# Kernel tuning notes

Hardware: AMD Instinct MI355X
Metric: run time of the kernel (lower is better)

The kernel has to match this reference:

```python
import jax, jax.numpy as jnp
import numpy as np

VOX = 64      # vox_size
KS = 21       # smooth_ks (odd -> 'SAME' == pad ks//2)
SIGMA = 3.0   # smooth_sigma


def smoothing_kernel():
    # normalized 1D gaussian used separably along the 3 voxel axes
    x = jnp.arange(KS, dtype=jnp.float32) - (KS - 1) / 2.0
    g = jnp.exp(-(x * x) / (2.0 * SIGMA * SIGMA))
    return g / g.sum()


def pc_voxels(pc, size):
    """Trilinear scatter of points in [-0.5,0.5]^3 into a [B,size,size,size] grid."""
    B, N, _ = pc.shape
    g = (pc + 0.5) * (size - 1)            # grid coords
    fl = jnp.floor(g)
    idx = fl.astype(jnp.int32)             # [B,N,3] lower corner
    frac = g - fl                          # trilinear fractions
    # 8 corner offsets in {0,1}^3
    offs = jnp.array([[(i >> 2) & 1, (i >> 1) & 1, i & 1] for i in range(8)], dtype=jnp.int32)
    pos = idx[:, :, None, :] + offs[None, None]                       # [B,N,8,3]
    w = jnp.prod(jnp.where(offs[None, None].astype(bool),
                           frac[:, :, None, :], 1.0 - frac[:, :, None, :]), axis=-1)  # [B,N,8]
    inb = jnp.all((pos >= 0) & (pos < size), axis=-1)
    w = jnp.where(inb, w, 0.0)
    posc = jnp.clip(pos, 0, size - 1)
    # voxel layout vox[b, z, y, x]; pc columns are (x, y, z)
    flat = posc[..., 2] * (size * size) + posc[..., 1] * size + posc[..., 0]
    vox = jnp.zeros((B, size * size * size), pc.dtype)
    vox = vox.at[jnp.arange(B)[:, None, None], flat].add(w)
    return jnp.clip(vox.reshape(B, size, size, size), 0.0, 1.0)


def voxels_smooth(v, g1d, scale):
    """Separable 3D Gaussian smoothing + per-batch scale, clamped to [0,1]."""
    x = v[:, None]  # NCDHW, C=1
    ks = g1d.shape[0]
    for kshape in ((1, 1, ks, 1, 1), (1, 1, 1, ks, 1), (1, 1, 1, 1, ks)):
        x = jax.lax.conv_general_dilated(
            x, g1d.reshape(kshape), (1, 1, 1), 'SAME',
            dimension_numbers=('NCDHW', 'OIDHW', 'NCDHW'))
    x = x[:, 0] * scale[:, None, None, None]
    return jnp.clip(x, 0.0, 1.0)


def drc_prob(v):
    """DRC ray-termination probabilities along depth (axis 1)."""
    trans = jnp.cumprod(1.0 - v, axis=1)                                   # [B,D,H,W]
    tshift = jnp.concatenate([jnp.ones_like(trans[:, :1]), trans[:, :-1]], axis=1)
    stop = v * tshift                                                      # stop at voxel d
    esc = trans[:, -1:]                                                    # ray escapes
    return jnp.concatenate([stop, esc], axis=1)                            # [B,D+1,H,W]


def reference(pc, rotation, scale):
    pc_t = jnp.einsum('bni,bji->bnj', pc, rotation)   # camera transform: pc @ R^T
    vox = pc_voxels(pc_t, VOX)
    sm = voxels_smooth(vox, smoothing_kernel(), scale)
    prob = drc_prob(sm)
    proj = prob[:, :-1].sum(1)[:, ::-1, :]            # sum over depth, flip rows
    return proj


def setup_inputs() -> dict:
    key = jax.random.key(0)
    k1, k2, k3 = jax.random.split(key, 3)
    B, N = 32, 65536
    pc = jax.random.uniform(k1, (B, N, 3), jnp.float32) - 0.5   # points in [-0.5, 0.5]
    q, _ = jnp.linalg.qr(jax.random.normal(k2, (B, 3, 3), jnp.float32))  # random rotations
    scale = 0.5 + jax.random.uniform(k3, (B,), jnp.float32)
    return {"pc": pc, "rotation": q, "scale": scale}
```

## Files before the change

kernel.cpp:

```cpp
#include <hip/hip_runtime.h>

#define NB    32
#define NP    65536
#define SZ    64
#define SZ3   (SZ * SZ * SZ)
#define KS    21
#define HALF  10
#define NBIN  65
#define CAP   2048
#define FXS   960.0f

typedef _Float16 half8_t __attribute__((ext_vector_type(8)));
typedef _Float16 half4_t __attribute__((ext_vector_type(4)));
typedef float    f32x4_t __attribute__((ext_vector_type(4)));

__device__ __forceinline__ int swz(int row, int col) {
    return (row << 6) + ((((col >> 3) ^ (row & 7))) << 3) + (col & 7);
}

__device__ __forceinline__ void weights_reg(float* w) {
    float sum = 0.0f;
#pragma unroll
    for (int k = 0; k < KS; ++k) {
        float d = (float)k - (float)HALF;
        w[k] = expf(-d * d / 18.0f);
        sum += w[k];
    }
#pragma unroll
    for (int k = 0; k < KS; ++k) w[k] /= sum;
}

__device__ __forceinline__ void fma4(float4& a, float t, const float4& v) {
    a.x = fmaf(t, v.x, a.x); a.y = fmaf(t, v.y, a.y);
    a.z = fmaf(t, v.z, a.z); a.w = fmaf(t, v.w, a.w);
}

__device__ __forceinline__ unsigned pack_fx(float g) {
    float c = fminf(fmaxf(g, -2.0f), 65.0f);
    return (unsigned)__float2uint_rn((c + 2.0f) * FXS);
}

__global__ void fill_kernel(const float* __restrict__ pc,
                            const float* __restrict__ rot,
                            int* __restrict__ cur,
                            uint2* __restrict__ binned,
                            _Float16* __restrict__ Gg) {
    __shared__ int h[4][NBIN];
    __shared__ int woff[4][NBIN];
    __shared__ int lbase[NBIN];
    int base = blockIdx.x * 1024;
    int b = base >> 16;
    int wv = threadIdx.x >> 6;
    for (int i = threadIdx.x; i < 4 * NBIN; i += 256) h[i / NBIN][i % NBIN] = 0;
    __syncthreads();
    const float* R = rot + b * 9;
    const float4* p4 = (const float4*)(pc + (size_t)base * 3);
    float4 f0 = p4[threadIdx.x * 3 + 0];
    float4 f1 = p4[threadIdx.x * 3 + 1];
    float4 f2 = p4[threadIdx.x * 3 + 2];
    float px[4] = {f0.x, f0.w, f1.z, f2.y};
    float py[4] = {f0.y, f1.x, f1.w, f2.z};
    float pz[4] = {f0.z, f1.y, f2.x, f2.w};
    uint2 pk[4];
    int bin[4], lpos[4];
#pragma unroll
    for (int j = 0; j < 4; ++j) {
        float g0 = (R[0] * px[j] + R[1] * py[j] + R[2] * pz[j] + 0.5f) * 63.0f;
        float g1 = (R[3] * px[j] + R[4] * py[j] + R[5] * pz[j] + 0.5f) * 63.0f;
        float g2 = (R[6] * px[j] + R[7] * py[j] + R[8] * pz[j] + 0.5f) * 63.0f;
        int i2 = (int)floorf(g2);
        bin[j] = (i2 >= -1 && i2 <= 63) ? i2 + 1 : -1;
        pk[j] = make_uint2(pack_fx(g0) | (pack_fx(g1) << 16), pack_fx(g2));
        if (bin[j] >= 0) lpos[j] = atomicAdd(&h[wv][bin[j]], 1);
    }
    __syncthreads();
    if (threadIdx.x < NBIN) {
        int t = threadIdx.x;
        int s0 = h[0][t], s1 = h[1][t], s2 = h[2][t], s3 = h[3][t];
        int tot = s0 + s1 + s2 + s3;
        lbase[t] = tot ? atomicAdd(&cur[b * NBIN + t], tot) : 0;
        woff[0][t] = 0; woff[1][t] = s0; woff[2][t] = s0 + s1; woff[3][t] = s0 + s1 + s2;
    }
    __syncthreads();
#pragma unroll
    for (int j = 0; j < 4; ++j)
        if (bin[j] >= 0) {
            int pos = lbase[bin[j]] + woff[wv][bin[j]] + lpos[j];
            if (pos < CAP)
                binned[(size_t)(b * NBIN + bin[j]) * CAP + pos] = pk[j];
        }
    if (blockIdx.x == 0) {
        float w[KS];
        weights_reg(w);
        for (int i = threadIdx.x; i < 4096; i += 256) {
            int d = (i >> 6) - (i & 63) + HALF;
            Gg[i] = ((unsigned)d < (unsigned)KS) ? (_Float16)w[d] : (_Float16)0.0f;
        }
    }
}

__global__ void __launch_bounds__(64) splat_blur(const uint2* __restrict__ binned,
                                                 const int* __restrict__ cur,
                                                 const _Float16* __restrict__ Gg,
                                                 _Float16* __restrict__ vox) {
    __shared__ __align__(16) _Float16 Ay[65 * 64];
    __shared__ __align__(16) _Float16 Bx[65 * 64];
    int lane = threadIdx.x;
    int idx = blockIdx.x;
    int b = idx >> 6;
    int z = (idx + (b << 3)) & 63;
    int q = lane >> 4, c = lane & 15;

    {
        int4 z4 = {0, 0, 0, 0};
        int4* a4 = (int4*)Ay;
        int4* b4 = (int4*)Bx;
        for (int i = lane; i < 65 * 64 * 2 / 16; i += 64) { a4[i] = z4; b4[i] = z4; }
    }

    half8_t gf[4][2];
#pragma unroll
    for (int ni = 0; ni < 4; ++ni)
#pragma unroll
        for (int h = 0; h < 2; ++h)
            gf[ni][h] = *(const half8_t*)&Gg[(ni * 16 + c) * 64 + h * 32 + q * 8];

    int c0 = min(cur[b * NBIN + z],     CAP);
    int c1 = min(cur[b * NBIN + z + 1], CAP);
    const uint2* s0 = binned + (size_t)(b * NBIN + z) * CAP;
    const uint2* s1 = binned + (size_t)(b * NBIN + z + 1) * CAP;
    int n = c0 + c1;

    f32x4_t acc[4][4];
#pragma unroll
    for (int mi = 0; mi < 4; ++mi)
#pragma unroll
        for (int ni = 0; ni < 4; ++ni) acc[mi][ni] = (f32x4_t){0.f, 0.f, 0.f, 0.f};

    int iters = (n + 63) >> 6;
    uint2 nxt = make_uint2(0u, 0u);
    if (lane < n) nxt = (lane < c0) ? s0[lane] : s1[lane - c0];
    for (int it = 0; it < iters; ++it) {
        uint2 pk = nxt;
        int ni2 = (it + 1) * 64 + lane;
        nxt = make_uint2(0u, 0u);
        if (ni2 < n) nxt = (ni2 < c0) ? s0[ni2] : s1[ni2 - c0];

        float gx = (float)(pk.x & 0xffffu) * (1.0f / FXS) - 2.0f;
        float gy = (float)(pk.x >> 16)     * (1.0f / FXS) - 2.0f;
        float gz = (float)(pk.y & 0xffffu) * (1.0f / FXS) - 2.0f;
        float f0 = floorf(gx), f1 = floorf(gy);
        int   i0 = (int)f0,    i1 = (int)f1;
        float r0 = gx - f0,    r1f = gy - f1;
        float az = fmaxf(0.0f, 1.0f - fabsf(gz - (float)z));
        int ylo = ((unsigned)i1       < 64u) ? i1       : 64;
        int yhi = ((unsigned)(i1 + 1) < 64u) ? (i1 + 1) : 64;
        int xlo = ((unsigned)i0       < 64u) ? i0       : 64;
        int xhi = ((unsigned)(i0 + 1) < 64u) ? (i0 + 1) : 64;
        Ay[swz(ylo, lane)] = (_Float16)(az * (1.0f - r1f));
        Ay[swz(yhi, lane)] = (_Float16)(az * r1f);
        Bx[swz(xlo, lane)] = (_Float16)(1.0f - r0);
        Bx[swz(xhi, lane)] = (_Float16)r0;
#pragma unroll
        for (int h = 0; h < 2; ++h) {
            half8_t af[4], bf[4];
#pragma unroll
            for (int mi = 0; mi < 4; ++mi)
                af[mi] = *(const half8_t*)&Ay[swz(mi * 16 + c, h * 32 + q * 8)];
#pragma unroll
            for (int ni = 0; ni < 4; ++ni)
                bf[ni] = *(const half8_t*)&Bx[swz(ni * 16 + c, h * 32 + q * 8)];
#pragma unroll
            for (int mi = 0; mi < 4; ++mi)
#pragma unroll
                for (int ni = 0; ni < 4; ++ni)
                    acc[mi][ni] = __builtin_amdgcn_mfma_f32_16x16x32_f16(
                        af[mi], bf[ni], acc[mi][ni], 0, 0, 0);
        }
        Ay[swz(ylo, lane)] = (_Float16)0.0f;
        Ay[swz(yhi, lane)] = (_Float16)0.0f;
        Bx[swz(xlo, lane)] = (_Float16)0.0f;
        Bx[swz(xhi, lane)] = (_Float16)0.0f;
    }

    asm volatile("" ::: "memory");
    _Float16* P = Ay;
    _Float16* T = Bx;

#pragma unroll
    for (int mi = 0; mi < 4; ++mi)
#pragma unroll
        for (int ni = 0; ni < 4; ++ni)
#pragma unroll
            for (int r = 0; r < 4; ++r)
                P[swz(mi * 16 + q * 4 + r, ni * 16 + c)] =
                    (_Float16)fminf(fmaxf(acc[mi][ni][r], 0.0f), 1.0f);
    asm volatile("" ::: "memory");

    f32x4_t a2[4][4];
#pragma unroll
    for (int mi = 0; mi < 4; ++mi)
#pragma unroll
        for (int ni = 0; ni < 4; ++ni) a2[mi][ni] = (f32x4_t){0.f, 0.f, 0.f, 0.f};
#pragma unroll
    for (int h = 0; h < 2; ++h) {
        half8_t af[4];
#pragma unroll
        for (int mi = 0; mi < 4; ++mi)
            af[mi] = *(const half8_t*)&P[swz(mi * 16 + c, h * 32 + q * 8)];
#pragma unroll
        for (int mi = 0; mi < 4; ++mi)
#pragma unroll
            for (int ni = 0; ni < 4; ++ni)
                a2[mi][ni] = __builtin_amdgcn_mfma_f32_16x16x32_f16(
                    af[mi], gf[ni][h], a2[mi][ni], 0, 0, 0);
    }
    asm volatile("" ::: "memory");

#pragma unroll
    for (int mi = 0; mi < 4; ++mi)
#pragma unroll
        for (int ni = 0; ni < 4; ++ni) {
            half4_t pkd;
#pragma unroll
            for (int r = 0; r < 4; ++r) pkd[r] = (_Float16)a2[mi][ni][r];
            *(half4_t*)&T[swz(ni * 16 + c, mi * 16 + q * 4)] = pkd;
        }
    asm volatile("" ::: "memory");

    f32x4_t a3[4][4];
#pragma unroll
    for (int mi = 0; mi < 4; ++mi)
#pragma unroll
        for (int ni = 0; ni < 4; ++ni) a3[mi][ni] = (f32x4_t){0.f, 0.f, 0.f, 0.f};
#pragma unroll
    for (int h = 0; h < 2; ++h) {
        half8_t bf[4];
#pragma unroll
        for (int ni = 0; ni < 4; ++ni)
            bf[ni] = *(const half8_t*)&T[swz(ni * 16 + c, h * 32 + q * 8)];
#pragma unroll
        for (int mi = 0; mi < 4; ++mi)
#pragma unroll
            for (int ni = 0; ni < 4; ++ni)
                a3[mi][ni] = __builtin_amdgcn_mfma_f32_16x16x32_f16(
                    gf[mi][h], bf[ni], a3[mi][ni], 0, 0, 0);
    }

    _Float16* dst = vox + ((size_t)b << 18) + ((size_t)z << 12);
#pragma unroll
    for (int mi = 0; mi < 4; ++mi)
#pragma unroll
        for (int ni = 0; ni < 4; ++ni)
#pragma unroll
            for (int r = 0; r < 4; ++r)
                dst[((mi * 16 + q * 4 + r) << 6) + ni * 16 + c] = (_Float16)a3[mi][ni][r];
}

__global__ void convz_drc_kernel(const _Float16* __restrict__ in,
                                 const float* __restrict__ scale,
                                 float* __restrict__ out) {
    __shared__ float sraw[640 + SZ * SZ + 640];
    __shared__ float c[SZ * SZ];
    __shared__ float segS[4][64], segT[4][64];
    float* s = sraw + 640;
    int b = blockIdx.x >> 6, y = blockIdx.x & 63;

    for (int i = threadIdx.x; i < 640; i += 256) {
        sraw[i] = 0.0f;
        sraw[640 + SZ * SZ + i] = 0.0f;
    }
    const _Float16* base = in + ((size_t)b << 18) + (y << 6);
#pragma unroll
    for (int g = 0; g < 4; ++g) {
        int cell = g * 256 + threadIdx.x;
        int z = cell >> 4, xc = (cell & 15) << 2;
        half4_t v = *(const half4_t*)&base[((size_t)z << 12) + xc];
        float4 f = make_float4((float)v[0], (float)v[1], (float)v[2], (float)v[3]);
        *(float4*)&s[(z << 6) + xc] = f;
    }
    __syncthreads();

    float w[KS];
    weights_reg(w);

    {
        int z0 = (threadIdx.x >> 4) << 2;
        int xc = (threadIdx.x & 15) << 2;
        float4 a0 = {0,0,0,0}, a1 = {0,0,0,0}, a2 = {0,0,0,0}, a3 = {0,0,0,0};
#pragma unroll
        for (int d = 0; d < 24; ++d) {
            int zz = z0 - HALF + d;
            float4 v = *(const float4*)&s[(zz << 6) + xc];
            if (d <= 20)           fma4(a0, w[d],     v);
            if (d >= 1 && d <= 21) fma4(a1, w[d - 1], v);
            if (d >= 2 && d <= 22) fma4(a2, w[d - 2], v);
            if (d >= 3)            fma4(a3, w[d - 3], v);
        }
        *(float4*)&c[((z0 + 0) << 6) + xc] = a0;
        *(float4*)&c[((z0 + 1) << 6) + xc] = a1;
        *(float4*)&c[((z0 + 2) << 6) + xc] = a2;
        *(float4*)&c[((z0 + 3) << 6) + xc] = a3;
    }
    __syncthreads();

    {
        int x = threadIdx.x & 63, seg = threadIdx.x >> 6;
        float sc = scale[b];
        float trans = 1.0f, sum = 0.0f;
#pragma unroll
        for (int zz = 0; zz < 16; ++zz) {
            int z = seg * 16 + zz;
            float v = fminf(fmaxf(c[(z << 6) + x] * sc, 0.0f), 1.0f);
            sum += v * trans;
            trans *= 1.0f - v;
        }
        segS[seg][x] = sum;
        segT[seg][x] = trans;
    }
    __syncthreads();
    if (threadIdx.x < 64) {
        int x = threadIdx.x;
        float t = 1.0f, S = 0.0f;
#pragma unroll
        for (int sgi = 0; sgi < 4; ++sgi) { S += segS[sgi][x] * t; t *= segT[sgi][x]; }
        out[(b << 12) + ((63 - y) << 6) + x] = S;
    }
}

extern "C" void kernel_launch(void* const* d_in, const int* in_sizes, int n_in,
                              void* d_out, int out_size, void* d_ws, size_t ws_size,
                              hipStream_t stream) {
    const float* pc    = (const float*)d_in[0];
    const float* rot   = (const float*)d_in[1];
    const float* scale = (const float*)d_in[2];
    float* out = (float*)d_out;

    _Float16* vox    = (_Float16*)d_ws;
    uint2*    binned = (uint2*)((char*)d_ws + (size_t)NB * SZ3 * sizeof(_Float16));
    _Float16* Gg     = (_Float16*)((char*)binned + (size_t)NB * NBIN * CAP * sizeof(uint2));
    int*      cur    = (int*)((char*)Gg + 64 * 64 * sizeof(_Float16));

    hipMemsetAsync(cur, 0, NB * NBIN * sizeof(int), stream);

    fill_kernel     <<<NB * NP / 1024, 256, 0, stream>>>(pc, rot, cur, binned, Gg);
    splat_blur      <<<NB * SZ, 64, 0, stream>>>(binned, cur, Gg, vox);
    convz_drc_kernel<<<NB * SZ, 256, 0, stream>>>(vox, scale, out);
}
```

Baseline: 126.2 us.

## Split splat_blur z-slice across two waves by binning points per y-half

Points are now binned by (z, y-half), so each z-slice block runs two wavefronts, each doing the splat MFMA outer-product over its 32-row half of y. The blur stages are split the same way and synchronised through shared memory. The change also deepens the point prefetch to two iterations and reorders z processing to start from the centre outwards. This trades duplicated binning of points that straddle the y=32 boundary and extra barriers for twice the wave parallelism and half the per-wave MFMA work in the serial splat loop. The smaller CAP2 raises overflow risk if bins are dense.

```diff
diff --git a/kernel.cpp b/kernel.cpp
--- a/kernel.cpp
+++ b/kernel.cpp
@@ -6,8 +6,8 @@
 #define SZ3   (SZ * SZ * SZ)
 #define KS    21
 #define HALF  10
-#define NBIN  65
-#define CAP   2048
+#define NBIN2 130
+#define CAP2  1280
 #define FXS   960.0f
 
 typedef _Float16 half8_t __attribute__((ext_vector_type(8)));
@@ -45,13 +45,13 @@
                             int* __restrict__ cur,
                             uint2* __restrict__ binned,
                             _Float16* __restrict__ Gg) {
-    __shared__ int h[4][NBIN];
-    __shared__ int woff[4][NBIN];
-    __shared__ int lbase[NBIN];
+    __shared__ int h[4][NBIN2];
+    __shared__ int woff[4][NBIN2];
+    __shared__ int lbase[NBIN2];
     int base = blockIdx.x * 1024;
     int b = base >> 16;
     int wv = threadIdx.x >> 6;
-    for (int i = threadIdx.x; i < 4 * NBIN; i += 256) h[i / NBIN][i % NBIN] = 0;
+    for (int i = threadIdx.x; i < 4 * NBIN2; i += 256) h[i / NBIN2][i % NBIN2] = 0;
     __syncthreads();
     const float* R = rot + b * 9;
     const float4* p4 = (const float4*)(pc + (size_t)base * 3);
@@ -62,33 +62,46 @@
     float py[4] = {f0.y, f1.x, f1.w, f2.z};
     float pz[4] = {f0.z, f1.y, f2.x, f2.w};
     uint2 pk[4];
-    int bin[4], lpos[4];
+    int bin0[4], bin1[4], lp0[4], lp1[4];
 #pragma unroll
     for (int j = 0; j < 4; ++j) {
         float g0 = (R[0] * px[j] + R[1] * py[j] + R[2] * pz[j] + 0.5f) * 63.0f;
         float g1 = (R[3] * px[j] + R[4] * py[j] + R[5] * pz[j] + 0.5f) * 63.0f;
         float g2 = (R[6] * px[j] + R[7] * py[j] + R[8] * pz[j] + 0.5f) * 63.0f;
         int i2 = (int)floorf(g2);
-        bin[j] = (i2 >= -1 && i2 <= 63) ? i2 + 1 : -1;
+        int i1 = (int)floorf(g1);
+        bool zv = (i2 >= -1 && i2 <= 63);
+        int h0 = ((unsigned)i1       < 64u) ? (i1 >> 5)       : -1;
+        int h1 = ((unsigned)(i1 + 1) < 64u) ? ((i1 + 1) >> 5) : -1;
+        if (h1 == h0) h1 = -1;
+        bin0[j] = (zv && h0 >= 0) ? ((i2 + 1) * 2 + h0) : -1;
+        bin1[j] = (zv && h1 >= 0) ? ((i2 + 1) * 2 + h1) : -1;
         pk[j] = make_uint2(pack_fx(g0) | (pack_fx(g1) << 16), pack_fx(g2));
-        if (bin[j] >= 0) lpos[j] = atomicAdd(&h[wv][bin[j]], 1);
-    }
-    __syncthreads();
-    if (threadIdx.x < NBIN) {
+        if (bin0[j] >= 0) lp0[j] = atomicAdd(&h[wv][bin0[j]], 1);
+        if (bin1[j] >= 0) lp1[j] = atomicAdd(&h[wv][bin1[j]], 1);
+    }
+    __syncthreads();
+    if (threadIdx.x < NBIN2) {
         int t = threadIdx.x;
         int s0 = h[0][t], s1 = h[1][t], s2 = h[2][t], s3 = h[3][t];
         int tot = s0 + s1 + s2 + s3;
-        lbase[t] = tot ? atomicAdd(&cur[b * NBIN + t], tot) : 0;
+        lbase[t] = tot ? atomicAdd(&cur[b * NBIN2 + t], tot) : 0;
         woff[0][t] = 0; woff[1][t] = s0; woff[2][t] = s0 + s1; woff[3][t] = s0 + s1 + s2;
     }
     __syncthreads();
 #pragma unroll
-    for (int j = 0; j < 4; ++j)
-        if (bin[j] >= 0) {
-            int pos = lbase[bin[j]] + woff[wv][bin[j]] + lpos[j];
-            if (pos < CAP)
-                binned[(size_t)(b * NBIN + bin[j]) * CAP + pos] = pk[j];
-        }
+    for (int j = 0; j < 4; ++j) {
+        if (bin0[j] >= 0) {
+            int pos = lbase[bin0[j]] + woff[wv][bin0[j]] + lp0[j];
+            if (pos < CAP2)
+                binned[(size_t)(b * NBIN2 + bin0[j]) * CAP2 + pos] = pk[j];
+        }
+        if (bin1[j] >= 0) {
+            int pos = lbase[bin1[j]] + woff[wv][bin1[j]] + lp1[j];
+            if (pos < CAP2)
+                binned[(size_t)(b * NBIN2 + bin1[j]) * CAP2 + pos] = pk[j];
+        }
+    }
     if (blockIdx.x == 0) {
         float w[KS];
         weights_reg(w);
@@ -99,52 +112,65 @@
     }
 }
 
-__global__ void __launch_bounds__(64) splat_blur(const uint2* __restrict__ binned,
-                                                 const int* __restrict__ cur,
-                                                 const _Float16* __restrict__ Gg,
-                                                 _Float16* __restrict__ vox) {
-    __shared__ __align__(16) _Float16 Ay[65 * 64];
-    __shared__ __align__(16) _Float16 Bx[65 * 64];
-    int lane = threadIdx.x;
+__global__ void __launch_bounds__(128) splat_blur(const uint2* __restrict__ binned,
+                                                  const int* __restrict__ cur,
+                                                  const _Float16* __restrict__ Gg,
+                                                  _Float16* __restrict__ vox) {
+    __shared__ __align__(16) char smem[25088];
+    int tid = threadIdx.x;
+    int w = tid >> 6, lane = tid & 63;
     int idx = blockIdx.x;
     int b = idx >> 6;
-    int z = (idx + (b << 3)) & 63;
+    int k = (idx + (b << 3)) & 63;
+    int z = (k & 1) ? (31 - (k >> 1)) : (32 + (k >> 1));
     int q = lane >> 4, c = lane & 15;
+
+    _Float16* Ay = (_Float16*)(smem + w * 4224);
+    _Float16* Bx = (_Float16*)(smem + 8448 + w * 8320);
+    _Float16* P  = (_Float16*)smem;
+    _Float16* T  = (_Float16*)(smem + 8448);
 
     {
         int4 z4 = {0, 0, 0, 0};
         int4* a4 = (int4*)Ay;
+        for (int i = lane; i < 4224 / 16; i += 64) a4[i] = z4;
         int4* b4 = (int4*)Bx;
-        for (int i = lane; i < 65 * 64 * 2 / 16; i += 64) { a4[i] = z4; b4[i] = z4; }
+        for (int i = lane; i < 8320 / 16; i += 64) b4[i] = z4;
     }
 
     half8_t gf[4][2];
 #pragma unroll
     for (int ni = 0; ni < 4; ++ni)
 #pragma unroll
-        for (int h = 0; h < 2; ++h)
-            gf[ni][h] = *(const half8_t*)&Gg[(ni * 16 + c) * 64 + h * 32 + q * 8];
-
-    int c0 = min(cur[b * NBIN + z],     CAP);
-    int c1 = min(cur[b * NBIN + z + 1], CAP);
-    const uint2* s0 = binned + (size_t)(b * NBIN + z) * CAP;
-    const uint2* s1 = binned + (size_t)(b * NBIN + z + 1) * CAP;
+        for (int hh = 0; hh < 2; ++hh)
+            gf[ni][hh] = *(const half8_t*)&Gg[(ni * 16 + c) * 64 + hh * 32 + q * 8];
+
+    int c0 = min(cur[b * NBIN2 + 2 * z + w],       CAP2);
+    int c1 = min(cur[b * NBIN2 + 2 * (z + 1) + w], CAP2);
+    const uint2* s0 = binned + (size_t)(b * NBIN2 + 2 * z + w) * CAP2;
+    const uint2* s1 = binned + (size_t)(b * NBIN2 + 2 * (z + 1) + w) * CAP2;
     int n = c0 + c1;
 
-    f32x4_t acc[4][4];
-#pragma unroll
-    for (int mi = 0; mi < 4; ++mi)
-#pragma unroll
-        for (int ni = 0; ni < 4; ++ni) acc[mi][ni] = (f32x4_t){0.f, 0.f, 0.f, 0.f};
+    f32x4_t acc[2][4];
+#pragma unroll
+    for (int ml = 0; ml < 2; ++ml)
+#pragma unroll
+        for (int ni = 0; ni < 4; ++ni) acc[ml][ni] = (f32x4_t){0.f, 0.f, 0.f, 0.f};
 
     int iters = (n + 63) >> 6;
-    uint2 nxt = make_uint2(0u, 0u);
-    if (lane < n) nxt = (lane < c0) ? s0[lane] : s1[lane - c0];
+    uint2 nxtA = make_uint2(0u, 0u), nxtB = make_uint2(0u, 0u);
+    {
+        int i0g = lane;
+        if (i0g < n) nxtA = (i0g < c0) ? s0[i0g] : s1[i0g - c0];
+        int i1g = 64 + lane;
+        if (i1g < n) nxtB = (i1g < c0) ? s0[i1g] : s1[i1g - c0];
+    }
     for (int it = 0; it < iters; ++it) {
-        uint2 pk = nxt;
-        int ni2 = (it + 1) * 64 + lane;
-        nxt = make_uint2(0u, 0u);
-        if (ni2 < n) nxt = (ni2 < c0) ? s0[ni2] : s1[ni2 - c0];
+        uint2 pk = nxtA;
+        nxtA = nxtB;
+        nxtB = make_uint2(0u, 0u);
+        int ni2 = (it + 2) * 64 + lane;
+        if (ni2 < n) nxtB = (ni2 < c0) ? s0[ni2] : s1[ni2 - c0];
 
         float gx = (float)(pk.x & 0xffffu) * (1.0f / FXS) - 2.0f;
         float gy = (float)(pk.x >> 16)     * (1.0f / FXS) - 2.0f;
@@ -153,108 +179,106 @@
         int   i0 = (int)f0,    i1 = (int)f1;
         float r0 = gx - f0,    r1f = gy - f1;
         float az = fmaxf(0.0f, 1.0f - fabsf(gz - (float)z));
-        int ylo = ((unsigned)i1       < 64u) ? i1       : 64;
-        int yhi = ((unsigned)(i1 + 1) < 64u) ? (i1 + 1) : 64;
+        int rlo = i1 - (w << 5), rhi = i1 + 1 - (w << 5);
+        int alo = ((unsigned)rlo < 32u) ? rlo : 32;
+        int ahi = ((unsigned)rhi < 32u) ? rhi : 32;
         int xlo = ((unsigned)i0       < 64u) ? i0       : 64;
         int xhi = ((unsigned)(i0 + 1) < 64u) ? (i0 + 1) : 64;
-        Ay[swz(ylo, lane)] = (_Float16)(az * (1.0f - r1f));
-        Ay[swz(yhi, lane)] = (_Float16)(az * r1f);
+        Ay[swz(alo, lane)] = (_Float16)(az * (1.0f - r1f));
+        Ay[swz(ahi, lane)] = (_Float16)(az * r1f);
         Bx[swz(xlo, lane)] = (_Float16)(1.0f - r0);
         Bx[swz(xhi, lane)] = (_Float16)r0;
 #pragma unroll
-        for (int h = 0; h < 2; ++h) {
-            half8_t af[4], bf[4];
-#pragma unroll
-            for (int mi = 0; mi < 4; ++mi)
-                af[mi] = *(const half8_t*)&Ay[swz(mi * 16 + c, h * 32 + q * 8)];
+        for (int hh = 0; hh < 2; ++hh) {
+            half8_t af[2], bf[4];
+#pragma unroll
+            for (int ml = 0; ml < 2; ++ml)
+                af[ml] = *(const half8_t*)&Ay[swz(ml * 16 + c, hh * 32 + q * 8)];
 #pragma unroll
             for (int ni = 0; ni < 4; ++ni)
-                bf[ni] = *(const half8_t*)&Bx[swz(ni * 16 + c, h * 32 + q * 8)];
-#pragma unroll
-            for (int mi = 0; mi < 4; ++mi)
+                bf[ni] = *(const half8_t*)&Bx[swz(ni * 16 + c, hh * 32 + q * 8)];
+#pragma unroll
+            for (int ml = 0; ml < 2; ++ml)
 #pragma unroll
                 for (int ni = 0; ni < 4; ++ni)
-                    acc[mi][ni] = __builtin_amdgcn_mfma_f32_16x16x32_f16(
-                        af[mi], bf[ni], acc[mi][ni], 0, 0, 0);
-        }
-        Ay[swz(ylo, lane)] = (_Float16)0.0f;
-        Ay[swz(yhi, lane)] = (_Float16)0.0f;
+                    acc[ml][ni] = __builtin_amdgcn_mfma_f32_16x16x32_f16(
+                        af[ml], bf[ni], acc[ml][ni], 0, 0, 0);
+        }
+        Ay[swz(alo, lane)] = (_Float16)0.0f;
+        Ay[swz(ahi, lane)] = (_Float16)0.0f;
         Bx[swz(xlo, lane)] = (_Float16)0.0f;
         Bx[swz(xhi, lane)] = (_Float16)0.0f;
     }
 
-    asm volatile("" ::: "memory");
-    _Float16* P = Ay;
-    _Float16* T = Bx;
-
-#pragma unroll
-    for (int mi = 0; mi < 4; ++mi)
+    __syncthreads();
+
+#pragma unroll
+    for (int ml = 0; ml < 2; ++ml)
 #pragma unroll
         for (int ni = 0; ni < 4; ++ni)
 #pragma unroll
             for (int r = 0; r < 4; ++r)
-                P[swz(mi * 16 + q * 4 + r, ni * 16 + c)] =
-                    (_Float16)fminf(fmaxf(acc[mi][ni][r], 0.0f), 1.0f);
-    asm volatile("" ::: "memory");
-
-    f32x4_t a2[4][4];
-#pragma unroll
-    for (int mi = 0; mi < 4; ++mi)
-#pragma unroll
-        for (int ni = 0; ni < 4; ++ni) a2[mi][ni] = (f32x4_t){0.f, 0.f, 0.f, 0.f};
-#pragma unroll
-    for (int h = 0; h < 2; ++h) {
-        half8_t af[4];
-#pragma unroll
-        for (int mi = 0; mi < 4; ++mi)
-            af[mi] = *(const half8_t*)&P[swz(mi * 16 + c, h * 32 + q * 8)];
-#pragma unroll
-        for (int mi = 0; mi < 4; ++mi)
+                P[swz((w << 5) + ml * 16 + q * 4 + r, ni * 16 + c)] =
+                    (_Float16)fminf(fmaxf(acc[ml][ni][r], 0.0f), 1.0f);
+    __syncthreads();
+
+    f32x4_t a2[2][4];
+#pragma unroll
+    for (int ml = 0; ml < 2; ++ml)
+#pragma unroll
+        for (int ni = 0; ni < 4; ++ni) a2[ml][ni] = (f32x4_t){0.f, 0.f, 0.f, 0.f};
+#pragma unroll
+    for (int hh = 0; hh < 2; ++hh) {
+        half8_t af[2];
+#pragma unroll
+        for (int ml = 0; ml < 2; ++ml)
+            af[ml] = *(const half8_t*)&P[swz(((w << 1) + ml) * 16 + c, hh * 32 + q * 8)];
+#pragma unroll
+        for (int ml = 0; ml < 2; ++ml)
 #pragma unroll
             for (int ni = 0; ni < 4; ++ni)
-                a2[mi][ni] = __builtin_amdgcn_mfma_f32_16x16x32_f16(
-                    af[mi], gf[ni][h], a2[mi][ni], 0, 0, 0);
-    }
-    asm volatile("" ::: "memory");
-
-#pragma unroll
-    for (int mi = 0; mi < 4; ++mi)
+                a2[ml][ni] = __builtin_amdgcn_mfma_f32_16x16x32_f16(
+                    af[ml], gf[ni][hh], a2[ml][ni], 0, 0, 0);
+    }
+#pragma unroll
+    for (int ml = 0; ml < 2; ++ml)
 #pragma unroll
         for (int ni = 0; ni < 4; ++ni) {
             half4_t pkd;
 #pragma unroll
-            for (int r = 0; r < 4; ++r) pkd[r] = (_Float16)a2[mi][ni][r];
-            *(half4_t*)&T[swz(ni * 16 + c, mi * 16 + q * 4)] = pkd;
-        }
-    asm volatile("" ::: "memory");
-
-    f32x4_t a3[4][4];
-#pragma unroll
-    for (int mi = 0; mi < 4; ++mi)
-#pragma unroll
-        for (int ni = 0; ni < 4; ++ni) a3[mi][ni] = (f32x4_t){0.f, 0.f, 0.f, 0.f};
-#pragma unroll
-    for (int h = 0; h < 2; ++h) {
+            for (int r = 0; r < 4; ++r) pkd[r] = (_Float16)a2[ml][ni][r];
+            *(half4_t*)&T[swz(ni * 16 + c, ((w << 1) + ml) * 16 + q * 4)] = pkd;
+        }
+    __syncthreads();
+
+    f32x4_t a3[2][4];
+#pragma unroll
+    for (int ml = 0; ml < 2; ++ml)
+#pragma unroll
+        for (int ni = 0; ni < 4; ++ni) a3[ml][ni] = (f32x4_t){0.f, 0.f, 0.f, 0.f};
+#pragma unroll
+    for (int hh = 0; hh < 2; ++hh) {
         half8_t bf[4];
 #pragma unroll
         for (int ni = 0; ni < 4; ++ni)
-            bf[ni] = *(const half8_t*)&T[swz(ni * 16 + c, h * 32 + q * 8)];
-#pragma unroll
-        for (int mi = 0; mi < 4; ++mi)
+            bf[ni] = *(const half8_t*)&T[swz(ni * 16 + c, hh * 32 + q * 8)];
+#pragma unroll
+        for (int ml = 0; ml < 2; ++ml)
 #pragma unroll
             for (int ni = 0; ni < 4; ++ni)
-                a3[mi][ni] = __builtin_amdgcn_mfma_f32_16x16x32_f16(
-                    gf[mi][h], bf[ni], a3[mi][ni], 0, 0, 0);
+                a3[ml][ni] = __builtin_amdgcn_mfma_f32_16x16x32_f16(
+                    gf[(w << 1) + ml][hh], bf[ni], a3[ml][ni], 0, 0, 0);
     }
 
     _Float16* dst = vox + ((size_t)b << 18) + ((size_t)z << 12);
 #pragma unroll
-    for (int mi = 0; mi < 4; ++mi)
+    for (int ml = 0; ml < 2; ++ml)
 #pragma unroll
         for (int ni = 0; ni < 4; ++ni)
 #pragma unroll
             for (int r = 0; r < 4; ++r)
-                dst[((mi * 16 + q * 4 + r) << 6) + ni * 16 + c] = (_Float16)a3[mi][ni][r];
+                dst[(((w << 5) + ml * 16 + q * 4 + r) << 6) + ni * 16 + c] =
+                    (_Float16)a3[ml][ni][r];
 }
 
 __global__ void convz_drc_kernel(const _Float16* __restrict__ in,
@@ -338,12 +362,12 @@
 
     _Float16* vox    = (_Float16*)d_ws;
     uint2*    binned = (uint2*)((char*)d_ws + (size_t)NB * SZ3 * sizeof(_Float16));
-    _Float16* Gg     = (_Float16*)((char*)binned + (size_t)NB * NBIN * CAP * sizeof(uint2));
+    _Float16* Gg     = (_Float16*)((char*)binned + (size_t)NB * NBIN2 * CAP2 * sizeof(uint2));
     int*      cur    = (int*)((char*)Gg + 64 * 64 * sizeof(_Float16));
 
-    hipMemsetAsync(cur, 0, NB * NBIN * sizeof(int), stream);
+    hipMemsetAsync(cur, 0, NB * NBIN2 * sizeof(int), stream);
 
     fill_kernel     <<<NB * NP / 1024, 256, 0, stream>>>(pc, rot, cur, binned, Gg);
-    splat_blur      <<<NB * SZ, 64, 0, stream>>>(binned, cur, Gg, vox);
+    splat_blur      <<<NB * SZ, 128, 0, stream>>>(binned, cur, Gg, vox);
     convz_drc_kernel<<<NB * SZ, 256, 0, stream>>>(vox, scale, out);
 }
```

Measured after the change: 123.8 us (median of 2 runs). No clear change (-1.9%).
